# Kernel tuning notes

Hardware: AMD Instinct MI355X
Metric: run time of the kernel (lower is better)

The kernel has to match this reference:

```python
import jax, jax.numpy as jnp
import numpy as np

CHUNK = 32


def l2norm(x):
    return x * jax.lax.rsqrt(jnp.sum(x * x, -1, keepdims=True) + 1e-6)


def causal_dwconv(x, w):
    # x: (b, l, C), w: (C, 1, k) -- depthwise causal 1D conv (left pad k-1)
    k = w.shape[-1]
    xt = jnp.transpose(x, (0, 2, 1))
    xt = jnp.pad(xt, ((0, 0), (0, 0), (k - 1, 0)))
    y = jax.lax.conv_general_dilated(xt, w, (1,), 'VALID',
                                     dimension_numbers=('NCH', 'OIH', 'NCH'),
                                     feature_group_count=xt.shape[1])
    return jnp.transpose(y, (0, 2, 1))


def delta_rule_chunkwise(q, k, v, beta):
    # q,k: (b,h,L,dk), v: (b,h,L,dv), beta: (b,h,L). L must be divisible by CHUNK.
    b, h, L, dk = q.shape
    dv = v.shape[-1]
    n = L // CHUNK
    q = l2norm(q)
    k = l2norm(k)
    v = v * beta[..., None]
    kb = k * beta[..., None]
    resh = lambda t: t.reshape(b, h, n, CHUNK, t.shape[-1])
    q, k, v, kb = (resh(t) for t in (q, k, v, kb))
    strict = jnp.tril(jnp.ones((CHUNK, CHUNK), bool), -1)
    A = jnp.where(strict, -(kb @ jnp.swapaxes(k, -1, -2)), 0.0)
    eye = jnp.eye(CHUNK, dtype=A.dtype)
    # UT transform: the sequential forward-substitution loop computes T = (I - A)^{-1}
    T = jax.scipy.linalg.solve_triangular(eye - A, jnp.broadcast_to(eye, A.shape), lower=True)
    u = T @ v
    w = T @ kb
    incl = jnp.tril(jnp.ones((CHUNK, CHUNK), bool))  # lower incl. diag

    def step(S, xs):
        q_i, k_i, u_i, w_i = xs
        attn = jnp.where(incl, q_i @ jnp.swapaxes(k_i, -1, -2), 0.0)
        u_hat = u_i - w_i @ S
        o_i = q_i @ S + attn @ u_hat
        return S + jnp.swapaxes(k_i, -1, -2) @ u_hat, o_i

    xs = tuple(jnp.moveaxis(t, 2, 0) for t in (q, k, u, w))
    S0 = jnp.zeros((b, h, dk, dv), q.dtype)
    S, o = jax.lax.scan(step, S0, xs)
    o = jnp.moveaxis(o, 0, 2).reshape(b, h, L, dv)
    return o, S


def branch_stats(x):
    # per-head stats over the feature dim: mean, std(ddof=1), mean|x|, L2 norm
    m = jnp.mean(x, -1, keepdims=True)
    s = jnp.std(x, -1, keepdims=True, ddof=1)
    a = jnp.mean(jnp.abs(x), -1, keepdims=True)
    l = jnp.sqrt(jnp.sum(x * x, -1, keepdims=True))
    return jnp.concatenate([m, s, a, l], -1)


def reference(hidden_states, q_w, k_w, v_w, b_w, qc_w, kc_w, vc_w,
              fir_w1, fir_w3, fir_w7, fir_w31,
              mlp_w1, mlp_b1, mlp_w2, mlp_b2, gate_log_temp, onorm_w, o_w):
    B, L, D = hidden_states.shape
    H = gate_log_temp.shape[0]
    dk = q_w.shape[1] // H
    dv = v_w.shape[1] // H
    # projections + causal short conv + silu
    q = jax.nn.silu(causal_dwconv(hidden_states @ q_w, qc_w))
    k = jax.nn.silu(causal_dwconv(hidden_states @ k_w, kc_w))
    v = jax.nn.silu(causal_dwconv(hidden_states @ v_w, vc_w))
    q = q.reshape(B, L, H, dk)
    k = k.reshape(B, L, H, dk)
    v_direct = v.reshape(B, L, H, dv)
    beta = jax.nn.sigmoid(hidden_states @ b_w)  # (B,L,H)
    delta_out, _ = delta_rule_chunkwise(
        jnp.transpose(q, (0, 2, 1, 3)), jnp.transpose(k, (0, 2, 1, 3)),
        jnp.transpose(v_direct, (0, 2, 1, 3)), jnp.transpose(beta, (0, 2, 1)))
    delta_out = jnp.transpose(delta_out, (0, 2, 1, 3))  # (B,L,H,dv)
    # multi-scale depthwise FIR branches on v
    v_flat = v_direct.reshape(B, L, H * dv)
    firs = [causal_dwconv(v_flat, w).reshape(B, L, H, dv)
            for w in (fir_w1, fir_w3, fir_w7, fir_w31)]
    branches = firs + [delta_out, v_direct]  # num_streams = 6
    S = len(branches)
    stats = jnp.concatenate([branch_stats(x) for x in branches], -1)  # (B,L,H,S*4)
    gate_in = jnp.concatenate([hidden_states, stats.reshape(B, L, H * S * 4)], -1)
    hgate = jax.nn.gelu(gate_in @ mlp_w1 + mlp_b1, approximate=False)
    logits = (hgate @ mlp_w2 + mlp_b2).reshape(B, L, H, S)
    temp = jax.nn.softplus(gate_log_temp) + 0.5  # min_gate_temp = 0.5
    weights = jax.nn.softmax(logits / temp[None, None, :, None], axis=-1)
    fused = sum(weights[..., i, None] * br for i, br in enumerate(branches))
    # RMSNorm over head_v_dim (eps=1e-5)
    fused = fused * jax.lax.rsqrt(jnp.mean(fused * fused, -1, keepdims=True) + 1e-5) * onorm_w
    return fused.reshape(B, L, H * dv) @ o_w


def setup_inputs() -> dict:
    key = jax.random.key(0)
    B, L, D, H = 2, 2048, 1024, 4
    dk = dv = D // H
    S = 6
    ks = iter(jax.random.split(key, 32))
    nrm = lambda shape, s=0.02: jax.random.normal(next(ks), shape, jnp.float32) * s

    def fir(kw):
        # delta init (last tap = 1) plus small noise
        base = jnp.zeros((H * dv, 1, kw), jnp.float32).at[:, 0, -1].set(1.0)
        return base + nrm((H * dv, 1, kw))

    gate_in_dim = D + S * 4 * H  # 1120
    hgd = D * 2 // 2             # 1024
    b2 = np.zeros(H * S, np.float32)
    for h in range(H):
        b2[h * S + S - 1] = 2.0  # value_bias_init on direct-value stream
    return {
        'hidden_states': jax.random.normal(next(ks), (B, L, D), jnp.float32),
        'q_w': nrm((D, D)), 'k_w': nrm((D, D)), 'v_w': nrm((D, D)),
        'b_w': nrm((D, H)),
        'qc_w': nrm((D, 1, 4), 0.3), 'kc_w': nrm((D, 1, 4), 0.3), 'vc_w': nrm((D, 1, 4), 0.3),
        'fir_w1': fir(1), 'fir_w3': fir(3), 'fir_w7': fir(7), 'fir_w31': fir(31),
        'mlp_w1': nrm((gate_in_dim, hgd)), 'mlp_b1': jnp.zeros((hgd,), jnp.float32),
        'mlp_w2': nrm((hgd, H * S)), 'mlp_b2': jnp.asarray(b2),
        'gate_log_temp': jnp.zeros((H,), jnp.float32),
        'onorm_w': jnp.ones((dv,), jnp.float32),
        'o_w': nrm((D, D)),
    }
```

## Files before the change

### kernel.cpp

```cpp
#include <hip/hip_runtime.h>
#include <hip/hip_bf16.h>
#include <math.h>

#define B_ 2
#define L_ 2048
#define D_ 1024
#define H_ 4
#define NC 64

typedef unsigned short ushort_t;
typedef __bf16 bf16x8 __attribute__((ext_vector_type(8)));
typedef float f32x4 __attribute__((ext_vector_type(4)));

__device__ __forceinline__ ushort_t f2bs(float f) {
    __hip_bfloat16 h = __float2bfloat16(f);
    ushort_t u;
    __builtin_memcpy(&u, &h, 2);
    return u;
}

__device__ __forceinline__ float wred(float v) {
    v += __shfl_down(v, 32);
    v += __shfl_down(v, 16);
    v += __shfl_down(v, 8);
    v += __shfl_down(v, 4);
    v += __shfl_down(v, 2);
    v += __shfl_down(v, 1);
    return v;
}

__device__ __forceinline__ void gload16(const void* g, void* l) {
    __builtin_amdgcn_global_load_lds((const __attribute__((address_space(1))) void*)g,
                                     (__attribute__((address_space(3))) void*)l, 16, 0, 0);
}

__global__ __launch_bounds__(256) void tcast_k(const float* __restrict__ W,
                                               ushort_t* __restrict__ WT, int K, int N) {
    __shared__ float tile[32 * 33];
    const int k0 = blockIdx.y << 5, n0 = blockIdx.x << 5;
    for (int e = threadIdx.x; e < 1024; e += 256)
        tile[(e >> 5) * 33 + (e & 31)] = W[(size_t)(k0 + (e >> 5)) * N + n0 + (e & 31)];
    __syncthreads();
    for (int e = threadIdx.x; e < 1024; e += 256)
        WT[(size_t)(n0 + (e >> 5)) * K + k0 + (e & 31)] = f2bs(tile[(e & 31) * 33 + (e >> 5)]);
}

__global__ __launch_bounds__(256) void cast_k(const float* __restrict__ x,
                                              ushort_t* __restrict__ y) {
    const int i = blockIdx.x * 256 + threadIdx.x;
    const float4 v = *(const float4*)&x[(size_t)i * 4];
    ushort4 p;
    p.x = f2bs(v.x); p.y = f2bs(v.y); p.z = f2bs(v.z); p.w = f2bs(v.w);
    *(ushort4*)&y[(size_t)i * 4] = p;
}

template <int ACT>
__global__ __launch_bounds__(256) void gemm_bf(const ushort_t* __restrict__ A,
                                               const ushort_t* __restrict__ Bt,
                                               const float* __restrict__ bias,
                                               float* __restrict__ C,
                                               int M, int N, int K) {
    __shared__ ushort_t As[128 * 32];
    __shared__ ushort_t Bs[128 * 32];
    const int t = threadIdx.x;
    const int wv = t >> 6, l = t & 63;
    const int m0 = blockIdx.y << 7, n0 = blockIdx.x << 7;
    const int wm = wv & 1, wn = wv >> 1;
    const int q4 = l >> 4, c16 = l & 15;
    f32x4 acc[4][4];
#pragma unroll
    for (int i = 0; i < 4; ++i)
#pragma unroll
        for (int j = 0; j < 4; ++j) {
            f32x4 z = {0.f, 0.f, 0.f, 0.f};
            acc[i][j] = z;
        }
    const int srow = (l >> 2);
    const int scol = (l & 3) << 3;
    for (int k0 = 0; k0 < K; k0 += 32) {
        __syncthreads();
#pragma unroll
        for (int si = 0; si < 2; ++si) {
            const int s = wv * 2 + si;
            gload16(&A[(size_t)(m0 + s * 16 + srow) * K + k0 + scol], &As[s * 512]);
            gload16(&Bt[(size_t)(n0 + s * 16 + srow) * K + k0 + scol], &Bs[s * 512]);
        }
        __syncthreads();
        bf16x8 af[4], bff[4];
#pragma unroll
        for (int mi = 0; mi < 4; ++mi)
            af[mi] = *(const bf16x8*)&As[(wm * 64 + mi * 16 + c16) * 32 + q4 * 8];
#pragma unroll
        for (int ni = 0; ni < 4; ++ni)
            bff[ni] = *(const bf16x8*)&Bs[(wn * 64 + ni * 16 + c16) * 32 + q4 * 8];
#pragma unroll
        for (int mi = 0; mi < 4; ++mi)
#pragma unroll
            for (int ni = 0; ni < 4; ++ni)
                acc[mi][ni] = __builtin_amdgcn_mfma_f32_16x16x32_bf16(af[mi], bff[ni],
                                                                     acc[mi][ni], 0, 0, 0);
    }
#pragma unroll
    for (int mi = 0; mi < 4; ++mi)
#pragma unroll
        for (int ni = 0; ni < 4; ++ni)
#pragma unroll
            for (int r = 0; r < 4; ++r) {
                const int row = m0 + wm * 64 + mi * 16 + q4 * 4 + r;
                const int col = n0 + wn * 64 + ni * 16 + c16;
                float v = acc[mi][ni][r];
                if (ACT == 1) {
                    v += bias[col];
                    v = 0.5f * v * (1.0f + erff(v * 0.70710678118654752f));
                }
                C[(size_t)row * N + col] = v;
            }
}

template <int DO_NORM, int EMIT_BF>
__global__ __launch_bounds__(256) void convql_k(const float* __restrict__ X,
                                                const float* __restrict__ cw,
                                                float* __restrict__ Y,
                                                ushort_t* __restrict__ Ybf) {
    __shared__ float xs[35 * 256];
    const int bid = blockIdx.x;
    const int h = bid & 3, lt = (bid >> 2) & 63, b = bid >> 8;
    const int t = threadIdx.x;
    const int l0 = lt << 5;
    const int cg = (h << 8) | t;
    for (int e = t; e < 35 * 256; e += 256) {
        const int r = e >> 8, c = e & 255;
        const int gl = l0 + r - 3;
        xs[e] = (gl >= 0) ? X[((size_t)(b * L_) + gl) * 3072 + (h << 8) + c] : 0.f;
    }
    const float w0 = cw[cg * 4 + 0], w1 = cw[cg * 4 + 1];
    const float w2 = cw[cg * 4 + 2], w3 = cw[cg * 4 + 3];
    __syncthreads();
    float yr[32];
#pragma unroll
    for (int l = 0; l < 32; ++l) {
        const float a = xs[(l + 0) * 256 + t] * w0 + xs[(l + 1) * 256 + t] * w1 +
                        xs[(l + 2) * 256 + t] * w2 + xs[(l + 3) * 256 + t] * w3;
        yr[l] = a / (1.f + expf(-a));
    }
    if (DO_NORM) {
        __syncthreads();
#pragma unroll
        for (int l = 0; l < 32; ++l) xs[l * 256 + t] = yr[l];
        __syncthreads();
        const int wv = t >> 6, lane = t & 63;
#pragma unroll
        for (int ri = 0; ri < 8; ++ri) {
            const int r = wv * 8 + ri;
            float4 v = *(float4*)&xs[r * 256 + lane * 4];
            float ss = v.x * v.x + v.y * v.y + v.z * v.z + v.w * v.w;
            ss = wred(ss);
            ss = __shfl(ss, 0);
            const float s = rsqrtf(ss + 1e-6f);
            v.x *= s; v.y *= s; v.z *= s; v.w *= s;
            const size_t go = ((size_t)(b * L_) + l0 + r) * 1024 + (h << 8) + lane * 4;
            *(float4*)&Y[go] = v;
            if (EMIT_BF) {
                ushort4 p;
                p.x = f2bs(v.x); p.y = f2bs(v.y); p.z = f2bs(v.z); p.w = f2bs(v.w);
                *(ushort4*)&Ybf[go] = p;
            }
        }
    } else {
#pragma unroll
        for (int l = 0; l < 32; ++l)
            Y[((size_t)(b * L_) + l0 + l) * 1024 + cg] = yr[l];
    }
}

__global__ __launch_bounds__(256) void fir_k(const float* __restrict__ V,
                                             const float* __restrict__ w1w,
                                             const float* __restrict__ w3w,
                                             const float* __restrict__ w7w,
                                             const float* __restrict__ w31w,
                                             float* __restrict__ o1,
                                             float* __restrict__ o3,
                                             float* __restrict__ o7,
                                             float* __restrict__ o31) {
    __shared__ float xs[62 * 256];
    const int bid = blockIdx.x;
    const int h = bid & 3, lt = (bid >> 2) & 63, b = bid >> 8;
    const int t = threadIdx.x;
    const int l0 = lt << 5;
    const int cg = (h << 8) | t;
    for (int e = t; e < 62 * 256; e += 256) {
        const int r = e >> 8, c = e & 255;
        const int gl = l0 + r - 30;
        xs[e] = (gl >= 0) ? V[((size_t)(b * L_) + gl) * 1024 + (h << 8) + c] : 0.f;
    }
    float lw31[31], lw7[7], lw3[3];
#pragma unroll
    for (int j = 0; j < 31; ++j) lw31[j] = w31w[cg * 31 + j];
#pragma unroll
    for (int j = 0; j < 7; ++j) lw7[j] = w7w[cg * 7 + j];
#pragma unroll
    for (int j = 0; j < 3; ++j) lw3[j] = w3w[cg * 3 + j];
    const float lw1 = w1w[cg];
    __syncthreads();
    for (int l = 0; l < 32; ++l) {
        float a31 = 0.f, a7 = 0.f, a3 = 0.f, v = 0.f;
#pragma unroll
        for (int j = 0; j < 31; ++j) {
            v = xs[(l + j) * 256 + t];
            a31 += v * lw31[j];
            if (j >= 24) a7 += v * lw7[j - 24];
            if (j >= 28) a3 += v * lw3[j - 28];
        }
        const size_t go = ((size_t)(b * L_) + l0 + l) * 1024 + cg;
        o31[go] = a31;
        o7[go] = a7;
        o3[go] = a3;
        o1[go] = v * lw1;
    }
}

__global__ __launch_bounds__(64) void beta_k(const float* __restrict__ hs,
                                             const float* __restrict__ bw,
                                             float* __restrict__ beta) {
    const int row = blockIdx.x;
    const int lane = threadIdx.x;
    float a0 = 0, a1 = 0, a2 = 0, a3 = 0;
    const float* hp = hs + (size_t)row * D_;
    for (int c = lane; c < D_; c += 64) {
        const float x = hp[c];
        a0 += x * bw[c * 4 + 0];
        a1 += x * bw[c * 4 + 1];
        a2 += x * bw[c * 4 + 2];
        a3 += x * bw[c * 4 + 3];
    }
    a0 = wred(a0); a1 = wred(a1); a2 = wred(a2); a3 = wred(a3);
    if (lane == 0) {
        float* o = beta + (size_t)row * 4;
        o[0] = 1.f / (1.f + expf(-a0));
        o[1] = 1.f / (1.f + expf(-a1));
        o[2] = 1.f / (1.f + expf(-a2));
        o[3] = 1.f / (1.f + expf(-a3));
    }
}

__global__ __launch_bounds__(256) void prep_k(const float* __restrict__ kg,
                                              const float* __restrict__ vg,
                                              const float* __restrict__ beta,
                                              ushort_t* __restrict__ wbf,
                                              float* __restrict__ ub) {
    __shared__ float lk[32 * 257];
    __shared__ float Am[32 * 33];
    __shared__ float Tm[32 * 33];
    __shared__ float lbeta[32];
    const int bid = blockIdx.x;
    const int bh = bid >> 6, ci = bid & 63;
    const int b = bh >> 2, h = bh & 3;
    const int t = threadIdx.x;
    const size_t gbase = ((size_t)(b * L_ + ci * 32)) * D_ + h * 256;
    for (int e = t; e < 8192; e += 256) {
        const int r = e >> 8, c = e & 255;
        lk[r * 257 + c] = kg[gbase + (size_t)r * D_ + c];
    }
    if (t < 32) lbeta[t] = beta[(size_t)(b * L_ + ci * 32 + t) * 4 + h];
    __syncthreads();
    for (int e = t; e < 1024; e += 256) {
        const int i = e >> 5, j = e & 31;
        float v = 0.f;
        if (j < i) {
            float d = 0.f;
            for (int c = 0; c < 256; ++c) d += lk[i * 257 + c] * lk[j * 257 + c];
            v = -lbeta[i] * d;
        }
        Am[i * 33 + j] = v;
        Tm[i * 33 + j] = (i == j) ? 1.f : 0.f;
    }
    __syncthreads();
    for (int i = 1; i < 32; ++i) {
        if (t < 32) {
            float s = 0.f;
            for (int j = 0; j < i; ++j) s += Am[i * 33 + j] * Tm[j * 33 + t];
            Tm[i * 33 + t] += s;
        }
        __syncthreads();
    }
    const size_t obase = (size_t)bid * 8192;
    for (int e = t; e < 8192; e += 256) {
        const int i = e >> 8, d = e & 255;
        float s = 0.f;
        for (int j = 0; j <= i; ++j) s += Tm[i * 33 + j] * lbeta[j] * lk[j * 257 + d];
        wbf[obase + e] = f2bs(s);
    }
    __syncthreads();
    for (int e = t; e < 8192; e += 256) {
        const int r = e >> 8, c = e & 255;
        lk[r * 257 + c] = vg[gbase + (size_t)r * D_ + c] * lbeta[r];
    }
    __syncthreads();
    for (int e = t; e < 8192; e += 256) {
        const int i = e >> 8, d = e & 255;
        float s = 0.f;
        for (int j = 0; j <= i; ++j) s += Tm[i * 33 + j] * lk[j * 257 + d];
        ub[obase + e] = s;
    }
}

__global__ __launch_bounds__(256) void attn_k(const float* __restrict__ qg,
                                              const float* __restrict__ kg,
                                              ushort_t* __restrict__ atg,
                                              ushort_t* __restrict__ ktg) {
    __shared__ float lk[32 * 257];
    const int bid = blockIdx.x;
    const int bh = bid >> 6, ci = bid & 63;
    const int b = bh >> 2, h = bh & 3;
    const int t = threadIdx.x;
    const size_t gbase = ((size_t)(b * L_ + ci * 32)) * D_ + h * 256;
    for (int e = t; e < 8192; e += 256) {
        const int r = e >> 8, c = e & 255;
        lk[r * 257 + c] = kg[gbase + (size_t)r * D_ + c];
    }
    __syncthreads();
    for (int e = t; e < 1024; e += 256) {
        const int i = e >> 5, j = e & 31;
        float v = 0.f;
        if (j <= i) {
            const float* qp = qg + gbase + (size_t)i * D_;
            for (int c = 0; c < 256; ++c) v += qp[c] * lk[j * 257 + c];
        }
        atg[(size_t)bid * 1024 + e] = f2bs(v);
    }
    for (int e = t; e < 8192; e += 256) {
        const int c = e >> 5, i = e & 31;
        ktg[(size_t)bid * 8192 + e] = f2bs(lk[i * 257 + c]);
    }
}

__global__ __launch_bounds__(256) void scan3_k(const ushort_t* __restrict__ qbf,
                                               const ushort_t* __restrict__ wbf,
                                               const float* __restrict__ ubuf,
                                               const ushort_t* __restrict__ atg,
                                               const ushort_t* __restrict__ ktg,
                                               float* __restrict__ dlt) {
    __shared__ ushort_t w_lds[32 * 256];
    __shared__ ushort_t q_lds[32 * 256];
    __shared__ ushort_t kT_lds[256 * 32];
    __shared__ ushort_t at_lds[32 * 32];
    __shared__ ushort_t uh_lds[16 * 40];
    __shared__ ushort_t S_lds[16 * 264];
    const int t = threadIdx.x;
    const int wv = t >> 6, lane = t & 63;
    const int bh = blockIdx.x & 7, tile = blockIdx.x >> 3;
    const int b = bh >> 2, h = bh & 3;
    const int l16 = lane & 15, quad = lane >> 4;
    for (int e = t; e < 16 * 264; e += 256) S_lds[e] = 0;

    auto stage = [&](int ci) {
        const size_t cb = (size_t)(bh * NC + ci);
        const ushort_t* wsrc = wbf + cb * 8192;
        const ushort_t* ksrc = ktg + cb * 8192;
        const ushort_t* asrc = atg + cb * 1024;
        const ushort_t* qsrc = qbf + ((size_t)(b * L_ + ci * 32)) * 1024 + (h << 8);
#pragma unroll
        for (int j = 0; j < 4; ++j) {
            const int blk = (wv << 2) + j;
            {
                const int r = (blk << 1) + (lane >> 5);
                const int sg = (lane & 31) ^ (r & 31);
                gload16(wsrc + r * 256 + (sg << 3), &w_lds[blk << 9]);
                gload16(qsrc + r * 1024 + (sg << 3), &q_lds[blk << 9]);
            }
            {
                const int r = (blk << 4) + (lane >> 2);
                const int sg = (lane & 3) ^ ((r >> 1) & 3);
                gload16(ksrc + (r << 5) + (sg << 3), &kT_lds[blk << 9]);
            }
        }
        if (wv < 2) {
            const int r = (wv << 4) + (lane >> 2);
            const int sg = (lane & 3) ^ ((r >> 1) & 3);
            gload16(asrc + (r << 5) + (sg << 3), &at_lds[wv << 9]);
        }
    };
    auto afrag = [&](const ushort_t* bb, int it, int k0) -> bf16x8 {
        const int i = (it << 4) + l16;
        const int s = (k0 >> 3) + quad;
        return *(const bf16x8*)&bb[(i << 8) + ((s ^ i) << 3)];
    };
    auto sfrag = [&](int k0) -> bf16x8 {
        return *(const bf16x8*)&S_lds[l16 * 264 + k0 + (quad << 3)];
    };
    auto ktfrag = [&](int tc) -> bf16x8 {
        const int c = (tc << 4) + l16;
        const int s = quad ^ ((c >> 1) & 3);
        return *(const bf16x8*)&kT_lds[(c << 5) + (s << 3)];
    };
    auto atfrag = [&](int it) -> bf16x8 {
        const int i = (it << 4) + l16;
        const int s = quad ^ ((i >> 1) & 3);
        return *(const bf16x8*)&at_lds[(i << 5) + (s << 3)];
    };
    auto uhfrag = [&]() -> bf16x8 {
        return *(const bf16x8*)&uh_lds[l16 * 40 + (quad << 3)];
    };

    f32x4 Sacc[8];
#pragma unroll
    for (int j = 0; j < 8; ++j) {
        f32x4 z = {0.f, 0.f, 0.f, 0.f};
        Sacc[j] = z;
    }
    stage(0);
    __syncthreads();
    for (int ci = 0; ci < NC; ++ci) {
        const size_t cb = (size_t)(bh * NC + ci);
        const size_t gbase = ((size_t)(b * L_ + ci * 32)) * D_ + (h << 8);
        if (wv < 2) {
            float uv[4];
#pragma unroll
            for (int r = 0; r < 4; ++r)
                uv[r] = ubuf[cb * 8192 + (size_t)((wv << 4) + (quad << 2) + r) * 256 +
                             (tile << 4) + l16];
            f32x4 acc = {0.f, 0.f, 0.f, 0.f};
#pragma unroll
            for (int k0 = 0; k0 < 256; k0 += 32)
                acc = __builtin_amdgcn_mfma_f32_16x16x32_bf16(afrag(w_lds, wv, k0),
                                                              sfrag(k0), acc, 0, 0, 0);
            ushort4 up;
            up.x = f2bs(uv[0] - acc[0]);
            up.y = f2bs(uv[1] - acc[1]);
            up.z = f2bs(uv[2] - acc[2]);
            up.w = f2bs(uv[3] - acc[3]);
            *(ushort4*)&uh_lds[l16 * 40 + (wv << 4) + (quad << 2)] = up;
        }
        __syncthreads();
        if (wv < 2) {
            f32x4 o = {0.f, 0.f, 0.f, 0.f};
#pragma unroll
            for (int k0 = 0; k0 < 256; k0 += 32)
                o = __builtin_amdgcn_mfma_f32_16x16x32_bf16(afrag(q_lds, wv, k0),
                                                            sfrag(k0), o, 0, 0, 0);
            o = __builtin_amdgcn_mfma_f32_16x16x32_bf16(atfrag(wv), uhfrag(), o, 0, 0, 0);
#pragma unroll
            for (int r = 0; r < 4; ++r)
                dlt[gbase + (size_t)((wv << 4) + (quad << 2) + r) * D_ + (tile << 4) + l16] =
                    o[r];
        } else {
            const int base_tc = (wv - 2) << 3;
            const bf16x8 uf = uhfrag();
#pragma unroll
            for (int j = 0; j < 8; ++j)
                Sacc[j] = __builtin_amdgcn_mfma_f32_16x16x32_bf16(ktfrag(base_tc + j), uf,
                                                                  Sacc[j], 0, 0, 0);
        }
        __syncthreads();
        if (ci + 1 < NC) stage(ci + 1);
        if (wv >= 2) {
            const int base_tc = (wv - 2) << 3;
#pragma unroll
            for (int j = 0; j < 8; ++j) {
                const int c0 = ((base_tc + j) << 4) + (quad << 2);
#pragma unroll
                for (int r = 0; r < 4; ++r)
                    S_lds[l16 * 264 + c0 + r] = f2bs(Sacc[j][r]);
            }
        }
        __syncthreads();
    }
}

__global__ __launch_bounds__(64) void stats_k(const float* __restrict__ f1,
                                              const float* __restrict__ f3,
                                              const float* __restrict__ f7,
                                              const float* __restrict__ f31,
                                              const float* __restrict__ dl,
                                              const float* __restrict__ vv,
                                              float* __restrict__ stat) {
    const int row = blockIdx.x;
    const int lane = threadIdx.x;
    const float* ptrs[6] = {f1, f3, f7, f31, dl, vv};
    const size_t base = (size_t)row * 256;
    for (int br = 0; br < 6; ++br) {
        const float4 x = *(const float4*)&ptrs[br][base + lane * 4];
        float s1 = x.x + x.y + x.z + x.w;
        float s2 = x.x * x.x + x.y * x.y + x.z * x.z + x.w * x.w;
        float sa = fabsf(x.x) + fabsf(x.y) + fabsf(x.z) + fabsf(x.w);
        s1 = wred(s1); s2 = wred(s2); sa = wred(sa);
        if (lane == 0) {
            const float m = s1 / 256.f;
            float var = (s2 - 256.f * m * m) / 255.f;
            if (var < 0.f) var = 0.f;
            float* o = &stat[(size_t)row * 24 + br * 4];
            o[0] = m;
            o[1] = sqrtf(var);
            o[2] = sa / 256.f;
            o[3] = sqrtf(s2);
        }
    }
}

__global__ __launch_bounds__(256) void gatein_k(const float* __restrict__ hs,
                                                const float* __restrict__ stat,
                                                ushort_t* __restrict__ gin) {
    const int idx = blockIdx.x * 256 + threadIdx.x;
    const int row = idx / 1120;
    const int j = idx - row * 1120;
    const float v = (j < 1024) ? hs[(size_t)row * 1024 + j]
                               : stat[(size_t)row * 96 + (j - 1024)];
    gin[idx] = f2bs(v);
}

__global__ __launch_bounds__(256) void wts_k(const float* __restrict__ hg,
                                             const float* __restrict__ w2,
                                             const float* __restrict__ b2,
                                             const float* __restrict__ glt,
                                             float* __restrict__ wts) {
    const int row = blockIdx.x;
    const int h = threadIdx.x >> 6, lane = threadIdx.x & 63;
    float hv[16];
    const float* hp = hg + (size_t)row * 1024;
#pragma unroll
    for (int ii = 0; ii < 16; ++ii) hv[ii] = hp[lane + 64 * ii];
    float lg[6];
#pragma unroll
    for (int s = 0; s < 6; ++s) {
        const int j = h * 6 + s;
        float acc = 0.f;
#pragma unroll
        for (int ii = 0; ii < 16; ++ii) acc += hv[ii] * w2[(size_t)(lane + 64 * ii) * 24 + j];
        lg[s] = wred(acc);
    }
    if (lane == 0) {
        const float temp = log1pf(expf(glt[h])) + 0.5f;
        float mx = -1e30f;
#pragma unroll
        for (int s = 0; s < 6; ++s) {
            lg[s] = (lg[s] + b2[h * 6 + s]) / temp;
            mx = fmaxf(mx, lg[s]);
        }
        float se = 0.f;
#pragma unroll
        for (int s = 0; s < 6; ++s) {
            lg[s] = expf(lg[s] - mx);
            se += lg[s];
        }
        float* o = &wts[(size_t)row * 24 + h * 6];
        const float inv = 1.f / se;
#pragma unroll
        for (int s = 0; s < 6; ++s) o[s] = lg[s] * inv;
    }
}

__global__ __launch_bounds__(1024) void fuse_k(const float* __restrict__ f1,
                                               const float* __restrict__ f3,
                                               const float* __restrict__ f7,
                                               const float* __restrict__ f31,
                                               const float* __restrict__ dl,
                                               const float* __restrict__ vv,
                                               const float* __restrict__ wts,
                                               const float* __restrict__ onw,
                                               ushort_t* __restrict__ fused) {
    __shared__ float wloc[24];
    __shared__ float psum[16];
    const int row = blockIdx.x, t = threadIdx.x;
    if (t < 24) wloc[t] = wts[(size_t)row * 24 + t];
    __syncthreads();
    const int h = t >> 8, dd = t & 255;
    const size_t idx = (size_t)row * 1024 + t;
    const float* ptrs[6] = {f1, f3, f7, f31, dl, vv};
    float f = 0.f;
#pragma unroll
    for (int br = 0; br < 6; ++br) f += wloc[h * 6 + br] * ptrs[br][idx];
    float ss = wred(f * f);
    const int wave = t >> 6;
    if ((t & 63) == 0) psum[wave] = ss;
    __syncthreads();
    const float tot = psum[h * 4 + 0] + psum[h * 4 + 1] + psum[h * 4 + 2] + psum[h * 4 + 3];
    const float scale = rsqrtf(tot / 256.f + 1e-5f);
    fused[idx] = f2bs(f * scale * onw[dd]);
}

extern "C" void kernel_launch(void* const* d_in, const int* in_sizes, int n_in,
                              void* d_out, int out_size, void* d_ws, size_t ws_size,
                              hipStream_t stream) {
    const float* hs   = (const float*)d_in[0];
    const float* q_w  = (const float*)d_in[1];
    const float* k_w  = (const float*)d_in[2];
    const float* v_w  = (const float*)d_in[3];
    const float* b_w  = (const float*)d_in[4];
    const float* qc_w = (const float*)d_in[5];
    const float* kc_w = (const float*)d_in[6];
    const float* vc_w = (const float*)d_in[7];
    const float* f1w  = (const float*)d_in[8];
    const float* f3w  = (const float*)d_in[9];
    const float* f7w  = (const float*)d_in[10];
    const float* f31w = (const float*)d_in[11];
    const float* w1   = (const float*)d_in[12];
    const float* b1   = (const float*)d_in[13];
    const float* w2   = (const float*)d_in[14];
    const float* b2   = (const float*)d_in[15];
    const float* glt  = (const float*)d_in[16];
    const float* onw  = (const float*)d_in[17];
    const float* o_w  = (const float*)d_in[18];
    float* out = (float*)d_out;

    const size_t SZ = (size_t)B_ * L_ * D_;
    float* qlin = (float*)d_ws;
    float* klin = qlin + SZ;
    float* vlin = klin + SZ;
    float* qbuf = vlin + SZ;
    float* kbuf = qbuf + SZ;
    float* vbuf = kbuf + SZ;
    float* f31b = vbuf + SZ;
    float* wb   = f31b + SZ;
    float* ub   = wb + SZ;
    float* dlt  = ub + SZ;
    float* beta = dlt + SZ;
    float* attn = beta + (size_t)B_ * L_ * H_;
    float* stat = attn + (size_t)B_ * H_ * NC * 1024;
    float* wts  = stat + (size_t)B_ * L_ * H_ * 24;
    float* f1b = qlin;
    float* f3b = klin;
    float* f7b = vlin;
    float* hgate = qbuf;
    float* qkv = qlin;

    ushort_t* hs_bf = (ushort_t*)dlt;
    ushort_t* qwT = (ushort_t*)f31b;
    ushort_t* kwT = (ushort_t*)f31b + 1048576;
    ushort_t* vwT = (ushort_t*)f31b + 2097152;
    ushort_t* qbf = (ushort_t*)f31b + 3145728;
    ushort_t* gin_bf = (ushort_t*)wb;
    ushort_t* w1T = (ushort_t*)(wb + 2359296);
    ushort_t* owT = (ushort_t*)ub;
    ushort_t* fused_bf = (ushort_t*)kbuf;
    ushort_t* ktg = (ushort_t*)klin;
    ushort_t* wbf = (ushort_t*)wb;
    ushort_t* at_bf = (ushort_t*)attn;

    const int M = B_ * L_;

    tcast_k<<<dim3(32, 32), 256, 0, stream>>>(q_w, qwT, 1024, 1024);
    tcast_k<<<dim3(32, 32), 256, 0, stream>>>(k_w, kwT, 1024, 1024);
    tcast_k<<<dim3(32, 32), 256, 0, stream>>>(v_w, vwT, 1024, 1024);
    cast_k<<<4096, 256, 0, stream>>>(hs, hs_bf);
    gemm_bf<0><<<dim3(24, 32), 256, 0, stream>>>(hs_bf, qwT, nullptr, qkv, M, 3072, 1024);
    beta_k<<<M, 64, 0, stream>>>(hs, b_w, beta);
    convql_k<1, 1><<<512, 256, 0, stream>>>(qkv + 0,    qc_w, qbuf, qbf);
    convql_k<1, 0><<<512, 256, 0, stream>>>(qkv + 1024, kc_w, kbuf, nullptr);
    convql_k<0, 0><<<512, 256, 0, stream>>>(qkv + 2048, vc_w, vbuf, nullptr);
    prep_k<<<B_ * H_ * NC, 256, 0, stream>>>(kbuf, vbuf, beta, wbf, ub);
    attn_k<<<B_ * H_ * NC, 256, 0, stream>>>(qbuf, kbuf, at_bf, ktg);
    scan3_k<<<128, 256, 0, stream>>>(qbf, wbf, ub, at_bf, ktg, dlt);
    fir_k<<<512, 256, 0, stream>>>(vbuf, f1w, f3w, f7w, f31w, f1b, f3b, f7b, f31b);
    stats_k<<<M * H_, 64, 0, stream>>>(f1b, f3b, f7b, f31b, dlt, vbuf, stat);
    gatein_k<<<17920, 256, 0, stream>>>(hs, stat, gin_bf);
    tcast_k<<<dim3(32, 35), 256, 0, stream>>>(w1, w1T, 1120, 1024);
    gemm_bf<1><<<dim3(8, 32), 256, 0, stream>>>(gin_bf, w1T, b1, hgate, M, 1024, 1120);
    wts_k<<<M, 256, 0, stream>>>(hgate, w2, b2, glt, wts);
    fuse_k<<<M, 1024, 0, stream>>>(f1b, f3b, f7b, f31b, dlt, vbuf, wts, onw, fused_bf);
    tcast_k<<<dim3(32, 32), 256, 0, stream>>>(o_w, owT, 1024, 1024);
    gemm_bf<0><<<dim3(8, 32), 256, 0, stream>>>(fused_bf, owT, nullptr, out, M, 1024, 1024);
}
```

Before: 636.1 us.

## Fuse prep/attn into MFMA prep kernel, register-prefetch scan, fold gate-input packing

Replaces the scalar fp32 prep_k and attn_k with a single prep2_k that computes the intra-chunk Gram, the causal q·k attention, and the T·k / T·v products using bf16 MFMA on bf16 q/k inputs. The scan kernel now double-buffers per-chunk fragments in registers instead of staging through LDS with global_load_lds, and uses lgkmcnt-wait barriers. The gate input is written directly by beta_k (the hs cast) and stats_k (the stats), removing gatein_k and the fp32 stat buffer, and fp32 q/k outputs from the conv are dropped. This cuts launches, global traffic and scalar FLOPs, at the cost of lower precision in A/T·v (bf16) and higher register pressure in the scan.

```diff
diff --git a/kernel.cpp b/kernel.cpp
--- a/kernel.cpp
+++ b/kernel.cpp
@@ -11,6 +11,7 @@
 typedef unsigned short ushort_t;
 typedef __bf16 bf16x8 __attribute__((ext_vector_type(8)));
 typedef float f32x4 __attribute__((ext_vector_type(4)));
+typedef ushort_t u16x8 __attribute__((ext_vector_type(8)));
 
 __device__ __forceinline__ ushort_t f2bs(float f) {
     __hip_bfloat16 h = __float2bfloat16(f);
@@ -33,6 +34,12 @@
     __builtin_amdgcn_global_load_lds((const __attribute__((address_space(1))) void*)g,
                                      (__attribute__((address_space(3))) void*)l, 16, 0, 0);
 }
+
+#define LGKM0_BAR()                                          \
+    do {                                                     \
+        asm volatile("s_waitcnt lgkmcnt(0)" ::: "memory");   \
+        __builtin_amdgcn_s_barrier();                        \
+    } while (0)
 
 __global__ __launch_bounds__(256) void tcast_k(const float* __restrict__ W,
                                                ushort_t* __restrict__ WT, int K, int N) {
@@ -117,7 +124,7 @@
             }
 }
 
-template <int DO_NORM, int EMIT_BF>
+template <int DO_NORM, int EMIT_F32, int EMIT_BF>
 __global__ __launch_bounds__(256) void convql_k(const float* __restrict__ X,
                                                 const float* __restrict__ cw,
                                                 float* __restrict__ Y,
@@ -159,7 +166,7 @@
             const float s = rsqrtf(ss + 1e-6f);
             v.x *= s; v.y *= s; v.z *= s; v.w *= s;
             const size_t go = ((size_t)(b * L_) + l0 + r) * 1024 + (h << 8) + lane * 4;
-            *(float4*)&Y[go] = v;
+            if (EMIT_F32) *(float4*)&Y[go] = v;
             if (EMIT_BF) {
                 ushort4 p;
                 p.x = f2bs(v.x); p.y = f2bs(v.y); p.z = f2bs(v.z); p.w = f2bs(v.w);
@@ -169,7 +176,7 @@
     } else {
 #pragma unroll
         for (int l = 0; l < 32; ++l)
-            Y[((size_t)(b * L_) + l0 + l) * 1024 + cg] = yr[l];
+            if (EMIT_F32) Y[((size_t)(b * L_) + l0 + l) * 1024 + cg] = yr[l];
     }
 }
 
@@ -221,13 +228,16 @@
 
 __global__ __launch_bounds__(64) void beta_k(const float* __restrict__ hs,
                                              const float* __restrict__ bw,
-                                             float* __restrict__ beta) {
+                                             float* __restrict__ beta,
+                                             ushort_t* __restrict__ gin) {
     const int row = blockIdx.x;
     const int lane = threadIdx.x;
     float a0 = 0, a1 = 0, a2 = 0, a3 = 0;
     const float* hp = hs + (size_t)row * D_;
+    ushort_t* gp = gin + (size_t)row * 1120;
     for (int c = lane; c < D_; c += 64) {
         const float x = hp[c];
+        gp[c] = f2bs(x);
         a0 += x * bw[c * 4 + 0];
         a1 += x * bw[c * 4 + 1];
         a2 += x * bw[c * 4 + 2];
@@ -243,36 +253,80 @@
     }
 }
 
-__global__ __launch_bounds__(256) void prep_k(const float* __restrict__ kg,
-                                              const float* __restrict__ vg,
-                                              const float* __restrict__ beta,
-                                              ushort_t* __restrict__ wbf,
-                                              float* __restrict__ ub) {
-    __shared__ float lk[32 * 257];
+__global__ __launch_bounds__(256) void prep2_k(const ushort_t* __restrict__ qbf,
+                                               const ushort_t* __restrict__ kbf,
+                                               const float* __restrict__ vg,
+                                               const float* __restrict__ beta,
+                                               ushort_t* __restrict__ wbf,
+                                               float* __restrict__ ub,
+                                               ushort_t* __restrict__ atg,
+                                               ushort_t* __restrict__ ktg) {
+    __shared__ ushort_t k_lds[32 * 264];
+    __shared__ ushort_t kT_lds[256 * 32];
+    __shared__ ushort_t vT_lds[256 * 32];
     __shared__ float Am[32 * 33];
     __shared__ float Tm[32 * 33];
-    __shared__ float lbeta[32];
+    __shared__ ushort_t Tb[32 * 40];
+    __shared__ float beta_s[32];
     const int bid = blockIdx.x;
     const int bh = bid >> 6, ci = bid & 63;
     const int b = bh >> 2, h = bh & 3;
     const int t = threadIdx.x;
-    const size_t gbase = ((size_t)(b * L_ + ci * 32)) * D_ + h * 256;
-    for (int e = t; e < 8192; e += 256) {
-        const int r = e >> 8, c = e & 255;
-        lk[r * 257 + c] = kg[gbase + (size_t)r * D_ + c];
-    }
-    if (t < 32) lbeta[t] = beta[(size_t)(b * L_ + ci * 32 + t) * 4 + h];
-    __syncthreads();
-    for (int e = t; e < 1024; e += 256) {
-        const int i = e >> 5, j = e & 31;
-        float v = 0.f;
-        if (j < i) {
-            float d = 0.f;
-            for (int c = 0; c < 256; ++c) d += lk[i * 257 + c] * lk[j * 257 + c];
-            v = -lbeta[i] * d;
-        }
-        Am[i * 33 + j] = v;
-        Tm[i * 33 + j] = (i == j) ? 1.f : 0.f;
+    const int wv = t >> 6, lane = t & 63;
+    const int l16 = lane & 15, quad = lane >> 4;
+    const size_t cb = (size_t)bid;
+    const size_t grow = ((size_t)(b * L_ + ci * 32)) * 1024 + (h << 8);
+    const f32x4 z4 = {0.f, 0.f, 0.f, 0.f};
+
+    if (t < 32) beta_s[t] = beta[(size_t)(b * L_ + ci * 32 + t) * 4 + h];
+#pragma unroll
+    for (int j = 0; j < 4; ++j) {
+        const int idx = j * 2048 + t * 8, r = idx >> 8, c = idx & 255;
+        *(u16x8*)&k_lds[r * 264 + c] = *(const u16x8*)&kbf[grow + (size_t)r * 1024 + c];
+    }
+#pragma unroll
+    for (int j = 0; j < 8; ++j) {
+        const int e = j * 1024 + t * 4, r = e >> 8, c = e & 255;
+        const float4 v4 = *(const float4*)&vg[grow + (size_t)r * 1024 + c];
+        const float vv[4] = {v4.x, v4.y, v4.z, v4.w};
+#pragma unroll
+        for (int x = 0; x < 4; ++x) {
+            const int cc = c + x;
+            const int sp = (r >> 3) ^ ((cc >> 1) & 3);
+            vT_lds[cc * 32 + sp * 8 + (r & 7)] = f2bs(vv[x]);
+        }
+    }
+    const int mi = wv & 1, ni = wv >> 1;
+    f32x4 g = z4, atv = z4;
+#pragma unroll
+    for (int s = 0; s < 8; ++s) {
+        const bf16x8 a =
+            *(const bf16x8*)&kbf[grow + (size_t)(mi * 16 + l16) * 1024 + s * 32 + (quad << 3)];
+        const bf16x8 bb =
+            *(const bf16x8*)&kbf[grow + (size_t)(ni * 16 + l16) * 1024 + s * 32 + (quad << 3)];
+        const bf16x8 qa =
+            *(const bf16x8*)&qbf[grow + (size_t)(mi * 16 + l16) * 1024 + s * 32 + (quad << 3)];
+        g = __builtin_amdgcn_mfma_f32_16x16x32_bf16(a, bb, g, 0, 0, 0);
+        atv = __builtin_amdgcn_mfma_f32_16x16x32_bf16(qa, bb, atv, 0, 0, 0);
+    }
+    __syncthreads();
+#pragma unroll
+    for (int r = 0; r < 4; ++r) {
+        const int row = mi * 16 + (quad << 2) + r;
+        const int col = ni * 16 + l16;
+        Am[row * 33 + col] = (col < row) ? -beta_s[row] * g[r] : 0.f;
+        Tm[row * 33 + col] = (row == col) ? 1.f : 0.f;
+        atg[cb * 1024 + row * 32 + col] = (col <= row) ? f2bs(atv[r]) : (ushort_t)0;
+    }
+#pragma unroll
+    for (int j = 0; j < 8; ++j) {
+        const int e = j * 1024 + t * 4, r = e >> 8, c = e & 255;
+#pragma unroll
+        for (int x = 0; x < 4; ++x) {
+            const int cc = c + x;
+            const int sp = (r >> 3) ^ ((cc >> 1) & 3);
+            kT_lds[cc * 32 + sp * 8 + (r & 7)] = k_lds[r * 264 + cc];
+        }
     }
     __syncthreads();
     for (int i = 1; i < 32; ++i) {
@@ -283,67 +337,44 @@
         }
         __syncthreads();
     }
-    const size_t obase = (size_t)bid * 8192;
-    for (int e = t; e < 8192; e += 256) {
-        const int i = e >> 8, d = e & 255;
-        float s = 0.f;
-        for (int j = 0; j <= i; ++j) s += Tm[i * 33 + j] * lbeta[j] * lk[j * 257 + d];
-        wbf[obase + e] = f2bs(s);
-    }
-    __syncthreads();
-    for (int e = t; e < 8192; e += 256) {
-        const int r = e >> 8, c = e & 255;
-        lk[r * 257 + c] = vg[gbase + (size_t)r * D_ + c] * lbeta[r];
-    }
-    __syncthreads();
-    for (int e = t; e < 8192; e += 256) {
-        const int i = e >> 8, d = e & 255;
-        float s = 0.f;
-        for (int j = 0; j <= i; ++j) s += Tm[i * 33 + j] * lk[j * 257 + d];
-        ub[obase + e] = s;
-    }
-}
-
-__global__ __launch_bounds__(256) void attn_k(const float* __restrict__ qg,
-                                              const float* __restrict__ kg,
-                                              ushort_t* __restrict__ atg,
-                                              ushort_t* __restrict__ ktg) {
-    __shared__ float lk[32 * 257];
-    const int bid = blockIdx.x;
-    const int bh = bid >> 6, ci = bid & 63;
-    const int b = bh >> 2, h = bh & 3;
-    const int t = threadIdx.x;
-    const size_t gbase = ((size_t)(b * L_ + ci * 32)) * D_ + h * 256;
-    for (int e = t; e < 8192; e += 256) {
-        const int r = e >> 8, c = e & 255;
-        lk[r * 257 + c] = kg[gbase + (size_t)r * D_ + c];
-    }
-    __syncthreads();
-    for (int e = t; e < 1024; e += 256) {
-        const int i = e >> 5, j = e & 31;
-        float v = 0.f;
-        if (j <= i) {
-            const float* qp = qg + gbase + (size_t)i * D_;
-            for (int c = 0; c < 256; ++c) v += qp[c] * lk[j * 257 + c];
-        }
-        atg[(size_t)bid * 1024 + e] = f2bs(v);
-    }
-    for (int e = t; e < 8192; e += 256) {
-        const int c = e >> 5, i = e & 31;
-        ktg[(size_t)bid * 8192 + e] = f2bs(lk[i * 257 + c]);
-    }
-}
-
-__global__ __launch_bounds__(256) void scan3_k(const ushort_t* __restrict__ qbf,
-                                               const ushort_t* __restrict__ wbf,
-                                               const float* __restrict__ ubuf,
-                                               const ushort_t* __restrict__ atg,
-                                               const ushort_t* __restrict__ ktg,
-                                               float* __restrict__ dlt) {
-    __shared__ ushort_t w_lds[32 * 256];
-    __shared__ ushort_t q_lds[32 * 256];
-    __shared__ ushort_t kT_lds[256 * 32];
-    __shared__ ushort_t at_lds[32 * 32];
+#pragma unroll
+    for (int j = 0; j < 4; ++j) {
+        const int e = j * 256 + t, i = e >> 5, jj = e & 31;
+        Tb[i * 40 + jj] = f2bs(Tm[i * 33 + jj] * beta_s[jj]);
+    }
+    __syncthreads();
+    const bf16x8 tf = *(const bf16x8*)&Tb[(mi * 16 + l16) * 40 + (quad << 3)];
+#pragma unroll
+    for (int j = 0; j < 8; ++j) {
+        const int nt = ni * 8 + j;
+        const int d = (nt << 4) + l16;
+        const int sp = quad ^ ((d >> 1) & 3);
+        const bf16x8 kb = *(const bf16x8*)&kT_lds[d * 32 + (sp << 3)];
+        const bf16x8 vb = *(const bf16x8*)&vT_lds[d * 32 + (sp << 3)];
+        const f32x4 wacc = __builtin_amdgcn_mfma_f32_16x16x32_bf16(tf, kb, z4, 0, 0, 0);
+        const f32x4 uacc = __builtin_amdgcn_mfma_f32_16x16x32_bf16(tf, vb, z4, 0, 0, 0);
+#pragma unroll
+        for (int r = 0; r < 4; ++r) {
+            const int row = mi * 16 + (quad << 2) + r;
+            wbf[cb * 8192 + row * 256 + d] = f2bs(wacc[r]);
+            ub[cb * 8192 + (size_t)row * 256 + d] = uacc[r];
+        }
+    }
+#pragma unroll
+    for (int j = 0; j < 4; ++j) {
+        const int idx = j * 2048 + t * 8;
+        const int c = idx >> 5, sl = (idx & 31) >> 3;
+        const int sp = sl ^ ((c >> 1) & 3);
+        *(u16x8*)&ktg[cb * 8192 + c * 32 + sl * 8] = *(const u16x8*)&kT_lds[c * 32 + sp * 8];
+    }
+}
+
+__global__ __launch_bounds__(256, 1) void scan4_k(const ushort_t* __restrict__ qbf,
+                                                  const ushort_t* __restrict__ wbf,
+                                                  const float* __restrict__ ubuf,
+                                                  const ushort_t* __restrict__ atg,
+                                                  const ushort_t* __restrict__ ktg,
+                                                  float* __restrict__ dlt) {
     __shared__ ushort_t uh_lds[16 * 40];
     __shared__ ushort_t S_lds[16 * 264];
     const int t = threadIdx.x;
@@ -353,77 +384,55 @@
     const int l16 = lane & 15, quad = lane >> 4;
     for (int e = t; e < 16 * 264; e += 256) S_lds[e] = 0;
 
-    auto stage = [&](int ci) {
+    f32x4 Sacc[8];
+#pragma unroll
+    for (int j = 0; j < 8; ++j) {
+        f32x4 z = {0.f, 0.f, 0.f, 0.f};
+        Sacc[j] = z;
+    }
+
+    bf16x8 wfA[8], qfA[8], atfA, ktA[8];
+    bf16x8 wfB[8], qfB[8], atfB, ktB[8];
+    float uvA[4], uvB[4];
+
+    auto loadf = [&](int ci, bf16x8* wf, bf16x8* qf, bf16x8& atf, float* uv, bf16x8* ktf) {
         const size_t cb = (size_t)(bh * NC + ci);
-        const ushort_t* wsrc = wbf + cb * 8192;
-        const ushort_t* ksrc = ktg + cb * 8192;
-        const ushort_t* asrc = atg + cb * 1024;
-        const ushort_t* qsrc = qbf + ((size_t)(b * L_ + ci * 32)) * 1024 + (h << 8);
-#pragma unroll
-        for (int j = 0; j < 4; ++j) {
-            const int blk = (wv << 2) + j;
-            {
-                const int r = (blk << 1) + (lane >> 5);
-                const int sg = (lane & 31) ^ (r & 31);
-                gload16(wsrc + r * 256 + (sg << 3), &w_lds[blk << 9]);
-                gload16(qsrc + r * 1024 + (sg << 3), &q_lds[blk << 9]);
+        if (wv < 2) {
+            const ushort_t* wsrc = wbf + cb * 8192;
+            const ushort_t* qsrc = qbf + ((size_t)(b * L_ + ci * 32)) * 1024 + (h << 8);
+            const int i = (wv << 4) + l16;
+#pragma unroll
+            for (int s = 0; s < 8; ++s) {
+                wf[s] = *(const bf16x8*)&wsrc[i * 256 + s * 32 + (quad << 3)];
+                qf[s] = *(const bf16x8*)&qsrc[(size_t)i * 1024 + s * 32 + (quad << 3)];
             }
-            {
-                const int r = (blk << 4) + (lane >> 2);
-                const int sg = (lane & 3) ^ ((r >> 1) & 3);
-                gload16(ksrc + (r << 5) + (sg << 3), &kT_lds[blk << 9]);
+            atf = *(const bf16x8*)&atg[cb * 1024 + i * 32 + (quad << 3)];
+#pragma unroll
+            for (int r = 0; r < 4; ++r)
+                uv[r] = ubuf[cb * 8192 + (size_t)((wv << 4) + (quad << 2) + r) * 256 +
+                             (tile << 4) + l16];
+        } else {
+            const ushort_t* ksrc = ktg + cb * 8192;
+#pragma unroll
+            for (int j = 0; j < 8; ++j) {
+                const int c = ((((wv - 2) << 3) + j) << 4) + l16;
+                ktf[j] = *(const bf16x8*)&ksrc[c * 32 + (quad << 3)];
             }
         }
-        if (wv < 2) {
-            const int r = (wv << 4) + (lane >> 2);
-            const int sg = (lane & 3) ^ ((r >> 1) & 3);
-            gload16(asrc + (r << 5) + (sg << 3), &at_lds[wv << 9]);
-        }
-    };
-    auto afrag = [&](const ushort_t* bb, int it, int k0) -> bf16x8 {
-        const int i = (it << 4) + l16;
-        const int s = (k0 >> 3) + quad;
-        return *(const bf16x8*)&bb[(i << 8) + ((s ^ i) << 3)];
     };
     auto sfrag = [&](int k0) -> bf16x8 {
         return *(const bf16x8*)&S_lds[l16 * 264 + k0 + (quad << 3)];
     };
-    auto ktfrag = [&](int tc) -> bf16x8 {
-        const int c = (tc << 4) + l16;
-        const int s = quad ^ ((c >> 1) & 3);
-        return *(const bf16x8*)&kT_lds[(c << 5) + (s << 3)];
-    };
-    auto atfrag = [&](int it) -> bf16x8 {
-        const int i = (it << 4) + l16;
-        const int s = quad ^ ((i >> 1) & 3);
-        return *(const bf16x8*)&at_lds[(i << 5) + (s << 3)];
-    };
     auto uhfrag = [&]() -> bf16x8 {
         return *(const bf16x8*)&uh_lds[l16 * 40 + (quad << 3)];
     };
-
-    f32x4 Sacc[8];
-#pragma unroll
-    for (int j = 0; j < 8; ++j) {
-        f32x4 z = {0.f, 0.f, 0.f, 0.f};
-        Sacc[j] = z;
-    }
-    stage(0);
-    __syncthreads();
-    for (int ci = 0; ci < NC; ++ci) {
-        const size_t cb = (size_t)(bh * NC + ci);
+    auto compute = [&](int ci, bf16x8* wf, bf16x8* qf, bf16x8& atf, float* uv, bf16x8* ktf) {
         const size_t gbase = ((size_t)(b * L_ + ci * 32)) * D_ + (h << 8);
         if (wv < 2) {
-            float uv[4];
-#pragma unroll
-            for (int r = 0; r < 4; ++r)
-                uv[r] = ubuf[cb * 8192 + (size_t)((wv << 4) + (quad << 2) + r) * 256 +
-                             (tile << 4) + l16];
             f32x4 acc = {0.f, 0.f, 0.f, 0.f};
 #pragma unroll
-            for (int k0 = 0; k0 < 256; k0 += 32)
-                acc = __builtin_amdgcn_mfma_f32_16x16x32_bf16(afrag(w_lds, wv, k0),
-                                                              sfrag(k0), acc, 0, 0, 0);
+            for (int s = 0; s < 8; ++s)
+                acc = __builtin_amdgcn_mfma_f32_16x16x32_bf16(wf[s], sfrag(s * 32), acc, 0, 0, 0);
             ushort4 up;
             up.x = f2bs(uv[0] - acc[0]);
             up.y = f2bs(uv[1] - acc[1]);
@@ -431,39 +440,43 @@
             up.w = f2bs(uv[3] - acc[3]);
             *(ushort4*)&uh_lds[l16 * 40 + (wv << 4) + (quad << 2)] = up;
         }
-        __syncthreads();
+        LGKM0_BAR();
         if (wv < 2) {
             f32x4 o = {0.f, 0.f, 0.f, 0.f};
 #pragma unroll
-            for (int k0 = 0; k0 < 256; k0 += 32)
-                o = __builtin_amdgcn_mfma_f32_16x16x32_bf16(afrag(q_lds, wv, k0),
-                                                            sfrag(k0), o, 0, 0, 0);
-            o = __builtin_amdgcn_mfma_f32_16x16x32_bf16(atfrag(wv), uhfrag(), o, 0, 0, 0);
+            for (int s = 0; s < 8; ++s)
+                o = __builtin_amdgcn_mfma_f32_16x16x32_bf16(qf[s], sfrag(s * 32), o, 0, 0, 0);
+            o = __builtin_amdgcn_mfma_f32_16x16x32_bf16(atf, uhfrag(), o, 0, 0, 0);
 #pragma unroll
             for (int r = 0; r < 4; ++r)
                 dlt[gbase + (size_t)((wv << 4) + (quad << 2) + r) * D_ + (tile << 4) + l16] =
                     o[r];
         } else {
-            const int base_tc = (wv - 2) << 3;
             const bf16x8 uf = uhfrag();
 #pragma unroll
             for (int j = 0; j < 8; ++j)
-                Sacc[j] = __builtin_amdgcn_mfma_f32_16x16x32_bf16(ktfrag(base_tc + j), uf,
-                                                                  Sacc[j], 0, 0, 0);
-        }
-        __syncthreads();
-        if (ci + 1 < NC) stage(ci + 1);
+                Sacc[j] = __builtin_amdgcn_mfma_f32_16x16x32_bf16(ktf[j], uf, Sacc[j], 0, 0, 0);
+        }
+        LGKM0_BAR();
         if (wv >= 2) {
-            const int base_tc = (wv - 2) << 3;
 #pragma unroll
             for (int j = 0; j < 8; ++j) {
-                const int c0 = ((base_tc + j) << 4) + (quad << 2);
+                const int c0 = ((((wv - 2) << 3) + j) << 4) + (quad << 2);
 #pragma unroll
                 for (int r = 0; r < 4; ++r)
                     S_lds[l16 * 264 + c0 + r] = f2bs(Sacc[j][r]);
             }
         }
-        __syncthreads();
+        LGKM0_BAR();
+    };
+
+    loadf(0, wfA, qfA, atfA, uvA, ktA);
+    LGKM0_BAR();
+    for (int ci = 0; ci < NC; ci += 2) {
+        loadf(ci + 1, wfB, qfB, atfB, uvB, ktB);
+        compute(ci, wfA, qfA, atfA, uvA, ktA);
+        if (ci + 2 < NC) loadf(ci + 2, wfA, qfA, atfA, uvA, ktA);
+        compute(ci + 1, wfB, qfB, atfB, uvB, ktB);
     }
 }
 
@@ -473,11 +486,12 @@
                                               const float* __restrict__ f31,
                                               const float* __restrict__ dl,
                                               const float* __restrict__ vv,
-                                              float* __restrict__ stat) {
+                                              ushort_t* __restrict__ gin) {
     const int row = blockIdx.x;
     const int lane = threadIdx.x;
     const float* ptrs[6] = {f1, f3, f7, f31, dl, vv};
     const size_t base = (size_t)row * 256;
+    ushort_t* gp = gin + (size_t)(row >> 2) * 1120 + 1024 + (row & 3) * 24;
     for (int br = 0; br < 6; ++br) {
         const float4 x = *(const float4*)&ptrs[br][base + lane * 4];
         float s1 = x.x + x.y + x.z + x.w;
@@ -488,24 +502,12 @@
             const float m = s1 / 256.f;
             float var = (s2 - 256.f * m * m) / 255.f;
             if (var < 0.f) var = 0.f;
-            float* o = &stat[(size_t)row * 24 + br * 4];
-            o[0] = m;
-            o[1] = sqrtf(var);
-            o[2] = sa / 256.f;
-            o[3] = sqrtf(s2);
-        }
-    }
-}
-
-__global__ __launch_bounds__(256) void gatein_k(const float* __restrict__ hs,
-                                                const float* __restrict__ stat,
-                                                ushort_t* __restrict__ gin) {
-    const int idx = blockIdx.x * 256 + threadIdx.x;
-    const int row = idx / 1120;
-    const int j = idx - row * 1120;
-    const float v = (j < 1024) ? hs[(size_t)row * 1024 + j]
-                               : stat[(size_t)row * 96 + (j - 1024)];
-    gin[idx] = f2bs(v);
+            gp[br * 4 + 0] = f2bs(m);
+            gp[br * 4 + 1] = f2bs(sqrtf(var));
+            gp[br * 4 + 2] = f2bs(sa / 256.f);
+            gp[br * 4 + 3] = f2bs(sqrtf(s2));
+        }
+    }
 }
 
 __global__ __launch_bounds__(256) void wts_k(const float* __restrict__ hg,
@@ -620,7 +622,7 @@
     float* f1b = qlin;
     float* f3b = klin;
     float* f7b = vlin;
-    float* hgate = qbuf;
+    float* hgate = kbuf;
     float* qkv = qlin;
 
     ushort_t* hs_bf = (ushort_t*)dlt;
@@ -628,13 +630,15 @@
     ushort_t* kwT = (ushort_t*)f31b + 1048576;
     ushort_t* vwT = (ushort_t*)f31b + 2097152;
     ushort_t* qbf = (ushort_t*)f31b + 3145728;
-    ushort_t* gin_bf = (ushort_t*)wb;
+    ushort_t* kbf = (ushort_t*)kbuf;
+    ushort_t* gin_bf = (ushort_t*)qbuf;
     ushort_t* w1T = (ushort_t*)(wb + 2359296);
     ushort_t* owT = (ushort_t*)ub;
     ushort_t* fused_bf = (ushort_t*)kbuf;
     ushort_t* ktg = (ushort_t*)klin;
     ushort_t* wbf = (ushort_t*)wb;
     ushort_t* at_bf = (ushort_t*)attn;
+    (void)stat;
 
     const int M = B_ * L_;
 
@@ -643,16 +647,14 @@
     tcast_k<<<dim3(32, 32), 256, 0, stream>>>(v_w, vwT, 1024, 1024);
     cast_k<<<4096, 256, 0, stream>>>(hs, hs_bf);
     gemm_bf<0><<<dim3(24, 32), 256, 0, stream>>>(hs_bf, qwT, nullptr, qkv, M, 3072, 1024);
-    beta_k<<<M, 64, 0, stream>>>(hs, b_w, beta);
-    convql_k<1, 1><<<512, 256, 0, stream>>>(qkv + 0,    qc_w, qbuf, qbf);
-    convql_k<1, 0><<<512, 256, 0, stream>>>(qkv + 1024, kc_w, kbuf, nullptr);
-    convql_k<0, 0><<<512, 256, 0, stream>>>(qkv + 2048, vc_w, vbuf, nullptr);
-    prep_k<<<B_ * H_ * NC, 256, 0, stream>>>(kbuf, vbuf, beta, wbf, ub);
-    attn_k<<<B_ * H_ * NC, 256, 0, stream>>>(qbuf, kbuf, at_bf, ktg);
-    scan3_k<<<128, 256, 0, stream>>>(qbf, wbf, ub, at_bf, ktg, dlt);
+    beta_k<<<M, 64, 0, stream>>>(hs, b_w, beta, gin_bf);
+    convql_k<1, 0, 1><<<512, 256, 0, stream>>>(qkv + 0,    qc_w, nullptr, qbf);
+    convql_k<1, 0, 1><<<512, 256, 0, stream>>>(qkv + 1024, kc_w, nullptr, kbf);
+    convql_k<0, 1, 0><<<512, 256, 0, stream>>>(qkv + 2048, vc_w, vbuf, nullptr);
+    prep2_k<<<B_ * H_ * NC, 256, 0, stream>>>(qbf, kbf, vbuf, beta, wbf, ub, at_bf, ktg);
+    scan4_k<<<128, 256, 0, stream>>>(qbf, wbf, ub, at_bf, ktg, dlt);
     fir_k<<<512, 256, 0, stream>>>(vbuf, f1w, f3w, f7w, f31w, f1b, f3b, f7b, f31b);
-    stats_k<<<M * H_, 64, 0, stream>>>(f1b, f3b, f7b, f31b, dlt, vbuf, stat);
-    gatein_k<<<17920, 256, 0, stream>>>(hs, stat, gin_bf);
+    stats_k<<<M * H_, 64, 0, stream>>>(f1b, f3b, f7b, f31b, dlt, vbuf, gin_bf);
     tcast_k<<<dim3(32, 35), 256, 0, stream>>>(w1, w1T, 1120, 1024);
     gemm_bf<1><<<dim3(8, 32), 256, 0, stream>>>(gin_bf, w1T, b1, hgate, M, 1024, 1120);
     wts_k<<<M, 256, 0, stream>>>(hgate, w2, b2, glt, wts);
```

Result: faster. 591.6 us (-7.0%).
